# Kernel tuning notes

Hardware: AMD Instinct MI355X
Metric: run time of the kernel (lower is better)

Reference implementation:

```python
import jax, jax.numpy as jnp
import numpy as np

N = 40960      # nodes, level 0
E = 327680     # edges, level 0
N1 = 20480     # nodes after first graclus pool
E2 = 163840    # edges after first pool
N2 = 10240     # nodes after second graclus pool
B = 512        # graphs in batch
NCLS = 10


def seg_mean(v, idx, n):
    s = jax.ops.segment_sum(v, idx, num_segments=n)
    c = jax.ops.segment_sum(jnp.ones((idx.shape[0], 1), v.dtype), idx, num_segments=n)
    return s / jnp.maximum(c, 1.0)


def seg_max_f(v, idx, n):
    m = jax.ops.segment_max(v, idx, num_segments=n)
    return jnp.where(jnp.isneginf(m), 0.0, m)  # empty clusters -> 0


def cartesian(pos, ei):
    # PyG T.Cartesian(): cart = pos[row]-pos[col], normalized to [0,1]
    cart = pos[ei[0]] - pos[ei[1]]
    m = jnp.max(jnp.abs(cart))
    return cart / (2.0 * m) + 0.5


def nnconv_mean(x, ei, eattr, w1, b1, w2, b2, root, bias, n_nodes):
    # edge MLP -> per-edge weight matrix [E, Fin, Fout]
    fin, fout = root.shape
    h = jax.nn.relu(eattr @ w1 + b1) @ w2 + b2
    W = h.reshape(-1, fin, fout)
    src, dst = ei[0], ei[1]
    msg = jnp.einsum('ei,eio->eo', x[src], W)          # gather + per-edge matmul
    aggr = seg_mean(msg, dst, n_nodes)                 # scatter-mean
    return x @ root + aggr + bias


def setup_inputs() -> dict:
    key = jax.random.key(0)
    ks = jax.random.split(key, 24)
    inp = {}
    inp['x'] = jax.random.normal(ks[0], (N, 1), jnp.float32)
    inp['pos'] = jax.random.uniform(ks[1], (N, 2), jnp.float32) * 28.0
    inp['edge_attr'] = jax.random.uniform(ks[2], (E, 2), jnp.float32)
    inp['edge_index'] = jax.random.randint(ks[3], (2, E), 0, N)
    inp['batch'] = jnp.sort(jax.random.randint(ks[4], (N,), 0, B))
    inp['cluster1'] = jax.random.randint(ks[5], (N,), 0, N1)
    inp['edge_index2'] = jax.random.randint(ks[6], (2, E2), 0, N1)
    inp['cluster2'] = jax.random.randint(ks[7], (N1,), 0, N2)
    s = 0.1
    inp['nn1_w1'] = jax.random.normal(ks[8], (2, 25), jnp.float32) * s
    inp['nn1_b1'] = jnp.zeros((25,), jnp.float32)
    inp['nn1_w2'] = jax.random.normal(ks[9], (25, 32), jnp.float32) * s
    inp['nn1_b2'] = jnp.zeros((32,), jnp.float32)
    inp['root1'] = jax.random.normal(ks[10], (1, 32), jnp.float32) * s
    inp['bias1'] = jnp.zeros((32,), jnp.float32)
    inp['nn2_w1'] = jax.random.normal(ks[11], (2, 25), jnp.float32) * s
    inp['nn2_b1'] = jnp.zeros((25,), jnp.float32)
    inp['nn2_w2'] = jax.random.normal(ks[12], (25, 2048), jnp.float32) * s
    inp['nn2_b2'] = jnp.zeros((2048,), jnp.float32)
    inp['root2'] = jax.random.normal(ks[13], (32, 64), jnp.float32) * s
    inp['bias2'] = jnp.zeros((64,), jnp.float32)
    inp['fc1_w'] = jax.random.normal(ks[14], (64, 128), jnp.float32) * s
    inp['fc1_b'] = jnp.zeros((128,), jnp.float32)
    inp['fc2_w'] = jax.random.normal(ks[15], (128, NCLS), jnp.float32) * s
    inp['fc2_b'] = jnp.zeros((NCLS,), jnp.float32)
    return inp


def reference(x, pos, edge_attr, edge_index, batch, cluster1, edge_index2, cluster2,
              nn1_w1, nn1_b1, nn1_w2, nn1_b2, root1, bias1,
              nn2_w1, nn2_b1, nn2_w2, nn2_b2, root2, bias2,
              fc1_w, fc1_b, fc2_w, fc2_b):
    # conv1 + ELU
    x1 = jax.nn.elu(nnconv_mean(x, edge_index, edge_attr,
                                nn1_w1, nn1_b1, nn1_w2, nn1_b2, root1, bias1, N))
    # graclus max_pool (clusters precomputed): max features, mean pos, pooled batch
    x1p = seg_max_f(x1, cluster1, N1)
    pos1 = seg_mean(pos, cluster1, N1)
    batch1 = jnp.clip(jax.ops.segment_max(batch, cluster1, num_segments=N1), 0, B - 1)
    eattr2 = cartesian(pos1, edge_index2)  # transform=Cartesian on pooled graph
    # conv2 + ELU
    x2 = jax.nn.elu(nnconv_mean(x1p, edge_index2, eattr2,
                                nn2_w1, nn2_b1, nn2_w2, nn2_b2, root2, bias2, N1))
    # max_pool_x then global_mean_pool
    x2p = seg_max_f(x2, cluster2, N2)
    batch2 = jnp.clip(jax.ops.segment_max(batch1, cluster2, num_segments=N2), 0, B - 1)
    xg = seg_mean(x2p, batch2, B)
    h = jax.nn.elu(xg @ fc1_w + fc1_b)
    # dropout is identity in eval mode
    logits = h @ fc2_w + fc2_b
    return jax.nn.log_softmax(logits, axis=1)
```

## Files before the change

kernel.cpp:

```cpp
#include <hip/hip_runtime.h>
#include <hip/hip_bf16.h>
#include <limits.h>

#define NN   40960
#define EE   327680
#define NN1  20480
#define EE2  163840
#define NN2  10240
#define BB   512
#define NCLS 10

#define SEG1 160
#define SEG2 240
#define SEG3 320
#define SEG4 400
#define SBT  440

typedef short bf16x8 __attribute__((ext_vector_type(8)));
typedef float f32x4 __attribute__((ext_vector_type(4)));

__device__ __forceinline__ float elu_f(float v) { return v > 0.f ? v : (expf(v) - 1.f); }
__device__ __forceinline__ unsigned f2bf_bits(float v) {
    unsigned u = __float_as_uint(v);
    return (u + 0x7FFFu + ((u >> 16) & 1u)) >> 16;
}

__global__ void init_all(int* zbase, int zcount) {
    int i = blockIdx.x * 256 + threadIdx.x;
    if (i < zcount) zbase[i] = 0;
}

__global__ void deg_count(const int* __restrict__ ei, const int* __restrict__ ei2,
                          const int* __restrict__ cluster1, const int* __restrict__ cluster2,
                          int* deg1, int* degS, int* degD, int* degC1, int* degC2) {
    int i = blockIdx.x * 256 + threadIdx.x;
    if (i < EE) atomicAdd(deg1 + ei[EE + i], 1);
    if (i < EE2) {
        atomicAdd(degS + ei2[i], 1);
        atomicAdd(degD + ei2[EE2 + i], 1);
    }
    if (i < NN) atomicAdd(degC1 + cluster1[i], 1);
    if (i < NN1) atomicAdd(degC2 + cluster2[i], 1);
}

__global__ __launch_bounds__(256) void scan_partial(
    const int* __restrict__ deg1, const int* __restrict__ degS,
    const int* __restrict__ degD, const int* __restrict__ degC1,
    const int* __restrict__ degC2, int* __restrict__ part) {
    int b = blockIdx.x, t = threadIdx.x;
    const int* src;
    int off;
    if (b < SEG1)      { src = deg1;  off = b * 256; }
    else if (b < SEG2) { src = degS;  off = (b - SEG1) * 256; }
    else if (b < SEG3) { src = degD;  off = (b - SEG2) * 256; }
    else if (b < SEG4) { src = degC1; off = (b - SEG3) * 256; }
    else               { src = degC2; off = (b - SEG4) * 256; }
    int v = src[off + t];
#pragma unroll
    for (int o = 32; o; o >>= 1) v += __shfl_down(v, o, 64);
    __shared__ int sred[4];
    if ((t & 63) == 0) sred[t >> 6] = v;
    __syncthreads();
    if (t == 0) part[b] = sred[0] + sred[1] + sred[2] + sred[3];
}

__global__ void scan_base(const int* __restrict__ part, int* __restrict__ partBase,
                          int* rowptr1, int* rowptrS, int* rowptrD,
                          int* rowptrC1, int* rowptrC2) {
    __shared__ int sh[SBT];
    int t = threadIdx.x;
    if (t < SBT) sh[t] = part[t];
    __syncthreads();
    if (t < 5) {
        int lo[6] = {0, SEG1, SEG2, SEG3, SEG4, SBT};
        int run = 0;
        for (int b = lo[t]; b < lo[t + 1]; b++) { int v = sh[b]; sh[b] = run; run += v; }
    }
    if (t == 5) {
        rowptr1[NN] = EE;
        rowptrS[NN1] = EE2;
        rowptrD[NN1] = EE2;
        rowptrC1[NN1] = NN;
        rowptrC2[NN2] = NN1;
    }
    __syncthreads();
    if (t < SBT) partBase[t] = sh[t];
}

__global__ __launch_bounds__(256) void scan_apply(
    const int* __restrict__ deg1, const int* __restrict__ degS,
    const int* __restrict__ degD, const int* __restrict__ degC1,
    const int* __restrict__ degC2, const int* __restrict__ partBase,
    int* rowptr1, int* rowptrS, int* rowptrD, int* rowptrC1, int* rowptrC2,
    int* cur1, int* curS, int* curD, int* curC1, int* curC2) {
    int b = blockIdx.x, t = threadIdx.x;
    const int* src;
    int *rp, *cur;
    int off;
    if (b < SEG1)      { src = deg1;  rp = rowptr1;  cur = cur1;  off = b * 256; }
    else if (b < SEG2) { src = degS;  rp = rowptrS;  cur = curS;  off = (b - SEG1) * 256; }
    else if (b < SEG3) { src = degD;  rp = rowptrD;  cur = curD;  off = (b - SEG2) * 256; }
    else if (b < SEG4) { src = degC1; rp = rowptrC1; cur = curC1; off = (b - SEG3) * 256; }
    else               { src = degC2; rp = rowptrC2; cur = curC2; off = (b - SEG4) * 256; }
    __shared__ int sh[256];
    int v = src[off + t];
    sh[t] = v;
    __syncthreads();
#pragma unroll
    for (int o = 1; o < 256; o <<= 1) {
        int u = (t >= o) ? sh[t - o] : 0;
        __syncthreads();
        sh[t] += u;
        __syncthreads();
    }
    int excl = sh[t] - v + partBase[b];
    rp[off + t] = excl;
    cur[off + t] = excl;
}

__global__ void fill_csr(const float* __restrict__ x, const float* __restrict__ ea,
                         const int* __restrict__ ei, const int* __restrict__ ei2,
                         const int* __restrict__ cluster1, const int* __restrict__ cluster2,
                         int* cur1, int* curS, int* curD, int* curC1, int* curC2,
                         float4* eadj1, int* cscDst, int* cscSrc, int* dstFrom,
                         int* memC1, int* memC2) {
    int i = blockIdx.x * 256 + threadIdx.x;
    if (i < EE) {
        int s = ei[i], d = ei[EE + i];
        int p = atomicAdd(cur1 + d, 1);
        eadj1[p] = make_float4(x[s], ea[2 * i], ea[2 * i + 1], 0.f);
    }
    if (i < EE2) {
        int s2 = ei2[i], d2 = ei2[EE2 + i];
        int q = atomicAdd(curS + s2, 1);
        cscDst[q] = d2;
        cscSrc[q] = s2;
        int p2 = atomicAdd(curD + d2, 1);
        dstFrom[p2] = q;
    }
    if (i < NN) {
        int c = cluster1[i];
        int p = atomicAdd(curC1 + c, 1);
        memC1[p] = i;
    }
    if (i < NN1) {
        int c = cluster2[i];
        int p = atomicAdd(curC2 + c, 1);
        memC2[p] = i;
    }
}

__global__ __launch_bounds__(256) void conv1_gather(
    const float* __restrict__ x, const int* __restrict__ rowptr1,
    const float4* __restrict__ eadj1,
    const float* __restrict__ w1, const float* __restrict__ b1,
    const float* __restrict__ w2, const float* __restrict__ b2,
    const float* __restrict__ root1, const float* __restrict__ bias1,
    float* __restrict__ x1) {
    int t = threadIdx.x;
    int j = t & 31;
    int n = blockIdx.x * 8 + (t >> 5);
    float w1x = 0.f, w1y = 0.f, b1j = 0.f;
    if (j < 25) { w1x = w1[j]; w1y = w1[25 + j]; b1j = b1[j]; }
    int r0 = rowptr1[n], r1 = rowptr1[n + 1];
    float agg = 0.f, sumx = 0.f;
    float4 edN = (r0 < r1) ? eadj1[r0] : make_float4(0.f, 0.f, 0.f, 0.f);
    for (int p = r0; p < r1; p++) {
        float4 ed = edN;
        if (p + 1 < r1) edN = eadj1[p + 1];
        float h = fmaxf(fmaf(ed.y, w1x, fmaf(ed.z, w1y, b1j)), 0.f);
        agg = fmaf(ed.x, h, agg);
        sumx += ed.x;
    }
    float w2c[25];
#pragma unroll
    for (int k = 0; k < 25; k++) w2c[k] = w2[k * 32 + j];
    float m = sumx * b2[j];
#pragma unroll
    for (int k = 0; k < 25; k++) m = fmaf(__shfl(agg, k, 32), w2c[k], m);
    float deg = fmaxf((float)(r1 - r0), 1.f);
    float v = fmaf(x[n], root1[j], m / deg + bias1[j]);
    x1[(size_t)n * 32 + j] = elu_f(v);
}

__global__ __launch_bounds__(256) void pool1_gather(
    const float* __restrict__ x1, const float* __restrict__ pos,
    const int* __restrict__ batch, const int* __restrict__ rowptrC1,
    const int* __restrict__ memC1,
    float* __restrict__ x1p, float* __restrict__ pos1, int* __restrict__ batch1) {
    int t = threadIdx.x;
    int j = t & 31;
    int c = blockIdx.x * 8 + (t >> 5);
    int r0 = rowptrC1[c], r1 = rowptrC1[c + 1];
    float mx = -INFINITY, sx = 0.f, sy = 0.f;
    int bmax = INT_MIN;
    for (int p = r0; p < r1; p++) {
        int v = memC1[p];
        mx = fmaxf(mx, x1[(size_t)v * 32 + j]);
        bmax = max(bmax, batch[v]);
        if (j == 0) {
            float2 pv = ((const float2*)pos)[v];
            sx += pv.x; sy += pv.y;
        }
    }
    x1p[(size_t)c * 32 + j] = (r0 < r1) ? mx : 0.f;
    if (j == 0) {
        float cn = fmaxf((float)(r1 - r0), 1.f);
        pos1[2 * c] = sx / cn;
        pos1[2 * c + 1] = sy / cn;
        batch1[c] = min(max(bmax, 0), BB - 1);
    }
}

__global__ void cartmax(const float* __restrict__ pos1, const int* __restrict__ ei2,
                        unsigned* mBits, const float* __restrict__ x1p,
                        unsigned short* __restrict__ x1pb) {
    int e = blockIdx.x * 256 + threadIdx.x;
#pragma unroll
    for (int u = 0; u < 4; u++) {
        int idx = e * 4 + u;
        x1pb[idx] = (unsigned short)f2bf_bits(x1p[idx]);
    }
    float m = 0.f;
    if (e < EE2) {
        int r = ei2[e], c = ei2[EE2 + e];
        m = fmaxf(fabsf(pos1[2 * r] - pos1[2 * c]), fabsf(pos1[2 * r + 1] - pos1[2 * c + 1]));
    }
    for (int off = 32; off; off >>= 1) m = fmaxf(m, __shfl_xor(m, off, 64));
    if ((threadIdx.x & 63) == 0) atomicMax(mBits, __float_as_uint(m));
}

__global__ void prep_wext(const float* __restrict__ w2, const float* __restrict__ b2,
                          unsigned short* __restrict__ WextB) {
    int idx = blockIdx.x * 256 + threadIdx.x;
    if (idx >= 13 * 8 * 64 * 8) return;
    int j = idx & 7;
    int lane = (idx >> 3) & 63;
    int tile = (idx >> 9) & 7;
    int ky = idx >> 12;
    int h = tile >> 2, tt = tile & 3;
    int kmlp = 2 * ky + h;
    int o = tt * 16 + (lane & 15);
    int i = (lane >> 4) * 8 + j;
    float v = (kmlp < 25) ? w2[(size_t)kmlp * 2048 + i * 64 + o] : b2[i * 64 + o];
    WextB[idx] = (unsigned short)f2bf_bits(v);
}

__global__ __launch_bounds__(256) void a_gemm_mfma(
    const unsigned short* __restrict__ x1pb, const unsigned short* __restrict__ WextB,
    unsigned* __restrict__ Au) {
    int t = threadIdx.x;
    int lane = t & 63;
    int w = t >> 6;
    int ky = blockIdx.y;
    int m0 = blockIdx.x * 128 + w * 32;
    int lo16 = lane & 15, hi4 = lane >> 4;
    bf16x8 bf[8];
    const bf16x8* Bp = (const bf16x8*)(WextB + (size_t)ky * 4096);
#pragma unroll
    for (int i = 0; i < 8; i++) bf[i] = Bp[i * 64 + lane];
    const f32x4 zero = {0.f, 0.f, 0.f, 0.f};
#pragma unroll
    for (int mt = 0; mt < 2; mt++) {
        int mbase = m0 + mt * 16;
        bf16x8 af = *(const bf16x8*)(x1pb + ((size_t)(mbase + lo16) * 32 + hi4 * 8));
        f32x4 acc[8];
#pragma unroll
        for (int i = 0; i < 8; i++)
            acc[i] = __builtin_amdgcn_mfma_f32_16x16x32_bf16(af, bf[i], zero, 0, 0, 0);
#pragma unroll
        for (int tt = 0; tt < 4; tt++) {
#pragma unroll
            for (int j = 0; j < 4; j++) {
                int n = mbase + hi4 * 4 + j;
                unsigned lo = f2bf_bits(acc[tt][j]);
                unsigned hi = f2bf_bits(acc[4 + tt][j]);
                Au[(size_t)n * 832 + ky * 64 + tt * 16 + lo16] = lo | (hi << 16);
            }
        }
    }
}

__global__ __launch_bounds__(256) void r2_kernel(
    const int* __restrict__ cscSrc, const int* __restrict__ cscDst,
    const float* __restrict__ pos1, const float* __restrict__ w1,
    const float* __restrict__ b1, const unsigned* __restrict__ mBits,
    unsigned* __restrict__ r2) {
    int q = blockIdx.x * 256 + threadIdx.x;
    if (q >= EE2) return;
    int s = cscSrc[q], d = cscDst[q];
    float inv = 0.5f / __uint_as_float(*mBits);
    float2 ps = ((const float2*)pos1)[s];
    float2 pd = ((const float2*)pos1)[d];
    float cx = fmaf(ps.x - pd.x, inv, 0.5f);
    float cy = fmaf(ps.y - pd.y, inv, 0.5f);
    unsigned out[13];
#pragma unroll
    for (int ky = 0; ky < 13; ky++) {
        int k0 = 2 * ky, k1 = 2 * ky + 1;
        float rlo = fmaxf(fmaf(cx, w1[k0], fmaf(cy, w1[25 + k0], b1[k0])), 0.f);
        float rhi = 1.f;
        if (k1 < 25) rhi = fmaxf(fmaf(cx, w1[k1], fmaf(cy, w1[25 + k1], b1[k1])), 0.f);
        out[ky] = f2bf_bits(rlo) | (f2bf_bits(rhi) << 16);
    }
#pragma unroll
    for (int ky = 0; ky < 13; ky++) r2[(size_t)q * 13 + ky] = out[ky];
}

__global__ __launch_bounds__(256) void conv2_msg(
    const unsigned* __restrict__ Au, const unsigned* __restrict__ r2,
    const int* __restrict__ rowptrS, unsigned short* __restrict__ msgbuf) {
    int t = threadIdx.x;
    int lane = t & 63;
    int s = __builtin_amdgcn_readfirstlane(blockIdx.x * 4 + (t >> 6));
    unsigned au[13];
    const unsigned* Ab = Au + (size_t)s * 832 + lane;
#pragma unroll
    for (int ky = 0; ky < 13; ky++) au[ky] = Ab[ky * 64];
    int r0 = rowptrS[s], r1 = rowptrS[s + 1];
    for (int q = r0; q < r1; q++) {
        const unsigned* rr = r2 + (size_t)q * 13;
        float m0 = 0.f, m1 = 0.f;
#pragma unroll
        for (int ky = 0; ky < 13; ky++) {
            unsigned rp = rr[ky];
            unsigned ua = au[ky];
            m0 = fmaf(__uint_as_float(rp << 16), __uint_as_float(ua << 16), m0);
            m1 = fmaf(__uint_as_float(rp & 0xFFFF0000u), __uint_as_float(ua & 0xFFFF0000u), m1);
        }
        msgbuf[(size_t)q * 64 + lane] = (unsigned short)f2bf_bits(m0 + m1);
    }
}

__global__ __launch_bounds__(256) void conv2_fin(
    const unsigned short* __restrict__ msgbuf, const int* __restrict__ rowptrD,
    const int* __restrict__ dstFrom,
    const float* __restrict__ x1p, const float* __restrict__ root2,
    const float* __restrict__ bias2, float* __restrict__ x2) {
    int t = threadIdx.x;
    int lane = t & 63;
    int n = blockIdx.x * 4 + (t >> 6);
    float Rr[32];
#pragma unroll
    for (int i = 0; i < 32; i++) Rr[i] = root2[i * 64 + lane];
    int r0 = rowptrD[n], r1 = rowptrD[n + 1];
    float acc = 0.f;
    int qN = (r0 < r1) ? dstFrom[r0] : 0;
    for (int p = r0; p < r1; p++) {
        int q = qN;
        if (p + 1 < r1) qN = dstFrom[p + 1];
        acc += __uint_as_float((unsigned)msgbuf[(size_t)q * 64 + lane] << 16);
    }
    float deg = fmaxf((float)(r1 - r0), 1.f);
    float xv = x1p[(size_t)n * 32 + (lane & 31)];
    float ra2 = bias2[lane];
#pragma unroll
    for (int i = 0; i < 32; i++) ra2 = fmaf(__shfl(xv, i, 64), Rr[i], ra2);
    x2[(size_t)n * 64 + lane] = elu_f(ra2 + acc / deg);
}

__global__ __launch_bounds__(256) void pool2_gather(
    const float* __restrict__ x2, const int* __restrict__ rowptrC2,
    const int* __restrict__ memC2, const int* __restrict__ batch1,
    float* __restrict__ xgsumS, float* __restrict__ gcntS) {
    int t = threadIdx.x;
    int lane = t & 63;
    int n2 = blockIdx.x * 4 + (t >> 6);
    int r0 = rowptrC2[n2], r1 = rowptrC2[n2 + 1];
    float mx = -INFINITY;
    int bmax = INT_MIN;
    for (int p = r0; p < r1; p++) {
        int m = memC2[p];
        mx = fmaxf(mx, x2[(size_t)m * 64 + lane]);
        bmax = max(bmax, batch1[m]);
    }
    float v = (r0 < r1) ? mx : 0.f;
    int b = min(max(bmax, 0), BB - 1);
    int shard = n2 & 7;
    atomicAdd(xgsumS + ((size_t)shard * BB + b) * 64 + lane, v);
    if (lane == 0) atomicAdd(gcntS + shard * BB + b, 1.f);
}

__global__ __launch_bounds__(128) void head_kernel(
    const float* __restrict__ xgsumS, const float* __restrict__ gcntS,
    const float* __restrict__ fc1w, const float* __restrict__ fc1b,
    const float* __restrict__ fc2w, const float* __restrict__ fc2b,
    float* __restrict__ out) {
    int b = blockIdx.x;
    int t = threadIdx.x;
    __shared__ float xg[64];
    __shared__ float h[128];
    __shared__ float lg[NCLS];
    __shared__ float red[2];
    __shared__ float cntsh;
    float s = 0.f;
    if (t < 64) {
#pragma unroll
        for (int sh = 0; sh < 8; sh++) s += xgsumS[((size_t)sh * BB + b) * 64 + t];
    }
    if (t == 64) {
        float c = 0.f;
#pragma unroll
        for (int sh = 0; sh < 8; sh++) c += gcntS[sh * BB + b];
        cntsh = fmaxf(c, 1.f);
    }
    __syncthreads();
    if (t < 64) xg[t] = s / cntsh;
    __syncthreads();
    float a1 = fc1b[t];
    for (int i = 0; i < 64; i++) a1 = fmaf(xg[i], fc1w[i * 128 + t], a1);
    h[t] = elu_f(a1);
    __syncthreads();
    if (t < NCLS) {
        float a = fc2b[t];
        for (int j = 0; j < 128; j++) a = fmaf(h[j], fc2w[j * NCLS + t], a);
        lg[t] = a;
    }
    __syncthreads();
    if (t == 0) {
        float mx = lg[0];
        for (int i = 1; i < NCLS; i++) mx = fmaxf(mx, lg[i]);
        float se = 0.f;
        for (int i = 0; i < NCLS; i++) se += expf(lg[i] - mx);
        red[0] = mx;
        red[1] = logf(se);
    }
    __syncthreads();
    if (t < NCLS) out[(size_t)b * NCLS + t] = lg[t] - red[0] - red[1];
}

extern "C" void kernel_launch(void* const* d_in, const int* in_sizes, int n_in,
                              void* d_out, int out_size, void* d_ws, size_t ws_size,
                              hipStream_t stream) {
    const float* x = (const float*)d_in[0];
    const float* pos = (const float*)d_in[1];
    const float* edge_attr = (const float*)d_in[2];
    const int* ei = (const int*)d_in[3];
    const int* batch = (const int*)d_in[4];
    const int* cluster1 = (const int*)d_in[5];
    const int* ei2 = (const int*)d_in[6];
    const int* cluster2 = (const int*)d_in[7];
    const float* nn1_w1 = (const float*)d_in[8];
    const float* nn1_b1 = (const float*)d_in[9];
    const float* nn1_w2 = (const float*)d_in[10];
    const float* nn1_b2 = (const float*)d_in[11];
    const float* root1 = (const float*)d_in[12];
    const float* bias1 = (const float*)d_in[13];
    const float* nn2_w1 = (const float*)d_in[14];
    const float* nn2_b1 = (const float*)d_in[15];
    const float* nn2_w2 = (const float*)d_in[16];
    const float* nn2_b2 = (const float*)d_in[17];
    const float* root2 = (const float*)d_in[18];
    const float* bias2 = (const float*)d_in[19];
    const float* fc1w = (const float*)d_in[20];
    const float* fc1b = (const float*)d_in[21];
    const float* fc2w = (const float*)d_in[22];
    const float* fc2b = (const float*)d_in[23];

    float* ws = (float*)d_ws;
    constexpr size_t OFF_DEG1 = 0;
    constexpr size_t OFF_DEGS = OFF_DEG1 + NN;
    constexpr size_t OFF_DEGD = OFF_DEGS + NN1;
    constexpr size_t OFF_DEGC1 = OFF_DEGD + NN1;
    constexpr size_t OFF_DEGC2 = OFF_DEGC1 + NN1;
    constexpr size_t OFF_XGS = OFF_DEGC2 + NN2;
    constexpr size_t OFF_GCS = OFF_XGS + (size_t)8 * BB * 64;
    constexpr size_t OFF_MBITS = OFF_GCS + 8 * BB;
    constexpr size_t ZTOT = OFF_MBITS + 1;
    constexpr size_t OFF_PART = ZTOT;
    constexpr size_t OFF_PBASE = OFF_PART + SBT;
    constexpr size_t OFF_ROWPTR1 = OFF_PBASE + SBT;
    constexpr size_t OFF_ROWPTRS = OFF_ROWPTR1 + NN + 4;
    constexpr size_t OFF_ROWPTRD = OFF_ROWPTRS + NN1 + 4;
    constexpr size_t OFF_ROWPTRC1 = OFF_ROWPTRD + NN1 + 4;
    constexpr size_t OFF_ROWPTRC2 = OFF_ROWPTRC1 + NN1 + 4;
    constexpr size_t OFF_CUR1 = OFF_ROWPTRC2 + NN2 + 4;
    constexpr size_t OFF_CURS = OFF_CUR1 + NN;
    constexpr size_t OFF_CURD = OFF_CURS + NN1;
    constexpr size_t OFF_CURC1 = OFF_CURD + NN1;
    constexpr size_t OFF_CURC2 = OFF_CURC1 + NN1;
    constexpr size_t OFF_CSCDST = OFF_CURC2 + NN2;
    constexpr size_t OFF_CSCSRC = OFF_CSCDST + EE2;
    constexpr size_t OFF_DSTFROM = OFF_CSCSRC + EE2;
    constexpr size_t OFF_MEMC1 = OFF_DSTFROM + EE2;
    constexpr size_t OFF_MEMC2 = OFF_MEMC1 + NN;
    constexpr size_t OFF_X1 = OFF_MEMC2 + NN1;
    constexpr size_t OFF_X1P = OFF_X1 + (size_t)NN * 32;
    constexpr size_t OFF_X1PB = OFF_X1P + (size_t)NN1 * 32;
    constexpr size_t OFF_POS1 = OFF_X1PB + (size_t)NN1 * 16;
    constexpr size_t OFF_BATCH1 = OFF_POS1 + (size_t)NN1 * 2;
    constexpr size_t OFF_X2 = OFF_BATCH1 + NN1;
    constexpr size_t OFF_WEXTB = OFF_X2 + (size_t)NN1 * 64;
    constexpr size_t OFF_UA = OFF_WEXTB + 26624;
    constexpr size_t UASZ = (size_t)EE2 * 13;
    constexpr size_t OFF_MSG = OFF_UA + UASZ;
    constexpr size_t OFF_AU = OFF_MSG + (size_t)EE2 * 32;

    int* deg1 = (int*)(ws + OFF_DEG1);
    int* degS = (int*)(ws + OFF_DEGS);
    int* degD = (int*)(ws + OFF_DEGD);
    int* degC1 = (int*)(ws + OFF_DEGC1);
    int* degC2 = (int*)(ws + OFF_DEGC2);
    float* xgsumS = ws + OFF_XGS;
    float* gcntS = ws + OFF_GCS;
    unsigned* mBits = (unsigned*)(ws + OFF_MBITS);
    int* part = (int*)(ws + OFF_PART);
    int* partBase = (int*)(ws + OFF_PBASE);
    int* rowptr1 = (int*)(ws + OFF_ROWPTR1);
    int* rowptrS = (int*)(ws + OFF_ROWPTRS);
    int* rowptrD = (int*)(ws + OFF_ROWPTRD);
    int* rowptrC1 = (int*)(ws + OFF_ROWPTRC1);
    int* rowptrC2 = (int*)(ws + OFF_ROWPTRC2);
    int* cur1 = (int*)(ws + OFF_CUR1);
    int* curS = (int*)(ws + OFF_CURS);
    int* curD = (int*)(ws + OFF_CURD);
    int* curC1 = (int*)(ws + OFF_CURC1);
    int* curC2 = (int*)(ws + OFF_CURC2);
    int* cscDst = (int*)(ws + OFF_CSCDST);
    int* cscSrc = (int*)(ws + OFF_CSCSRC);
    int* dstFrom = (int*)(ws + OFF_DSTFROM);
    int* memC1 = (int*)(ws + OFF_MEMC1);
    int* memC2 = (int*)(ws + OFF_MEMC2);
    float* x1 = ws + OFF_X1;
    float* x1p = ws + OFF_X1P;
    unsigned short* x1pb = (unsigned short*)(ws + OFF_X1PB);
    float* pos1 = ws + OFF_POS1;
    int* batch1 = (int*)(ws + OFF_BATCH1);
    float* x2 = ws + OFF_X2;
    unsigned short* WextB = (unsigned short*)(ws + OFF_WEXTB);
    float4* eadj1 = (float4*)(ws + OFF_UA);
    unsigned* r2 = (unsigned*)(ws + OFF_UA);
    unsigned short* msgbuf = (unsigned short*)(ws + OFF_MSG);
    unsigned* Au = (unsigned*)(ws + OFF_AU);

    init_all<<<(int)((ZTOT + 255) / 256), 256, 0, stream>>>((int*)d_ws, (int)ZTOT);
    deg_count<<<EE / 256, 256, 0, stream>>>(ei, ei2, cluster1, cluster2,
                                            deg1, degS, degD, degC1, degC2);
    scan_partial<<<SBT, 256, 0, stream>>>(deg1, degS, degD, degC1, degC2, part);
    scan_base<<<1, 512, 0, stream>>>(part, partBase, rowptr1, rowptrS, rowptrD,
                                     rowptrC1, rowptrC2);
    scan_apply<<<SBT, 256, 0, stream>>>(deg1, degS, degD, degC1, degC2, partBase,
                                        rowptr1, rowptrS, rowptrD, rowptrC1, rowptrC2,
                                        cur1, curS, curD, curC1, curC2);
    fill_csr<<<EE / 256, 256, 0, stream>>>(x, edge_attr, ei, ei2, cluster1, cluster2,
                                           cur1, curS, curD, curC1, curC2,
                                           eadj1, cscDst, cscSrc, dstFrom, memC1, memC2);
    prep_wext<<<208, 256, 0, stream>>>(nn2_w2, nn2_b2, WextB);
    conv1_gather<<<NN / 8, 256, 0, stream>>>(x, rowptr1, eadj1,
                                             nn1_w1, nn1_b1, nn1_w2, nn1_b2, root1, bias1, x1);
    pool1_gather<<<NN1 / 8, 256, 0, stream>>>(x1, pos, batch, rowptrC1, memC1,
                                              x1p, pos1, batch1);
    cartmax<<<EE2 / 256, 256, 0, stream>>>(pos1, ei2, mBits, x1p, x1pb);
    a_gemm_mfma<<<dim3(NN1 / 128, 13), 256, 0, stream>>>(x1pb, WextB, Au);
    r2_kernel<<<EE2 / 256, 256, 0, stream>>>(cscSrc, cscDst, pos1, nn2_w1, nn2_b1, mBits, r2);
    conv2_msg<<<NN1 / 4, 256, 0, stream>>>(Au, r2, rowptrS, msgbuf);
    conv2_fin<<<NN1 / 4, 256, 0, stream>>>(msgbuf, rowptrD, dstFrom, x1p, root2, bias2, x2);
    pool2_gather<<<NN2 / 4, 256, 0, stream>>>(x2, rowptrC2, memC2, batch1, xgsumS, gcntS);
    head_kernel<<<BB, 128, 0, stream>>>(xgsumS, gcntS, fc1w, fc1b, fc2w, fc2b,
                                        (float*)d_out);
}
```

Measured before the change: 245.7 us.

## Record atomic slots in degree pass, scatter messages directly in dst order

The degree-count kernel now saves each element's atomic return value as its slot, so CSR fill becomes a plain rowptr+slot write with no second round of atomics and no cursor arrays. Edge source, destination and destination position are packed into one int4 record, and the per-edge r2 row is padded to 16 words so it can be read with vector loads and carry the destination slot. conv2_msg then writes messages straight into destination order, which removes the dstFrom indirection in conv2_fin. In exchange it adds slot arrays and padding that raise memory traffic, and the message writes become scattered instead of sequential.

New measurement: 208.9 us. -15.0%, faster.

```diff
diff --git a/kernel.cpp b/kernel.cpp
--- a/kernel.cpp
+++ b/kernel.cpp
@@ -32,15 +32,16 @@
 
 __global__ void deg_count(const int* __restrict__ ei, const int* __restrict__ ei2,
                           const int* __restrict__ cluster1, const int* __restrict__ cluster2,
-                          int* deg1, int* degS, int* degD, int* degC1, int* degC2) {
+                          int* deg1, int* degS, int* degD, int* degC1, int* degC2,
+                          int* slot1, int* slotS, int* slotD, int* slotC1, int* slotC2) {
     int i = blockIdx.x * 256 + threadIdx.x;
-    if (i < EE) atomicAdd(deg1 + ei[EE + i], 1);
+    if (i < EE) slot1[i] = atomicAdd(deg1 + ei[EE + i], 1);
     if (i < EE2) {
-        atomicAdd(degS + ei2[i], 1);
-        atomicAdd(degD + ei2[EE2 + i], 1);
-    }
-    if (i < NN) atomicAdd(degC1 + cluster1[i], 1);
-    if (i < NN1) atomicAdd(degC2 + cluster2[i], 1);
+        slotS[i] = atomicAdd(degS + ei2[i], 1);
+        slotD[i] = atomicAdd(degD + ei2[EE2 + i], 1);
+    }
+    if (i < NN) slotC1[i] = atomicAdd(degC1 + cluster1[i], 1);
+    if (i < NN1) slotC2[i] = atomicAdd(degC2 + cluster2[i], 1);
 }
 
 __global__ __launch_bounds__(256) void scan_partial(
@@ -91,17 +92,16 @@
     const int* __restrict__ deg1, const int* __restrict__ degS,
     const int* __restrict__ degD, const int* __restrict__ degC1,
     const int* __restrict__ degC2, const int* __restrict__ partBase,
-    int* rowptr1, int* rowptrS, int* rowptrD, int* rowptrC1, int* rowptrC2,
-    int* cur1, int* curS, int* curD, int* curC1, int* curC2) {
+    int* rowptr1, int* rowptrS, int* rowptrD, int* rowptrC1, int* rowptrC2) {
     int b = blockIdx.x, t = threadIdx.x;
     const int* src;
-    int *rp, *cur;
+    int* rp;
     int off;
-    if (b < SEG1)      { src = deg1;  rp = rowptr1;  cur = cur1;  off = b * 256; }
-    else if (b < SEG2) { src = degS;  rp = rowptrS;  cur = curS;  off = (b - SEG1) * 256; }
-    else if (b < SEG3) { src = degD;  rp = rowptrD;  cur = curD;  off = (b - SEG2) * 256; }
-    else if (b < SEG4) { src = degC1; rp = rowptrC1; cur = curC1; off = (b - SEG3) * 256; }
-    else               { src = degC2; rp = rowptrC2; cur = curC2; off = (b - SEG4) * 256; }
+    if (b < SEG1)      { src = deg1;  rp = rowptr1;  off = b * 256; }
+    else if (b < SEG2) { src = degS;  rp = rowptrS;  off = (b - SEG1) * 256; }
+    else if (b < SEG3) { src = degD;  rp = rowptrD;  off = (b - SEG2) * 256; }
+    else if (b < SEG4) { src = degC1; rp = rowptrC1; off = (b - SEG3) * 256; }
+    else               { src = degC2; rp = rowptrC2; off = (b - SEG4) * 256; }
     __shared__ int sh[256];
     int v = src[off + t];
     sh[t] = v;
@@ -113,41 +113,33 @@
         sh[t] += u;
         __syncthreads();
     }
-    int excl = sh[t] - v + partBase[b];
-    rp[off + t] = excl;
-    cur[off + t] = excl;
+    rp[off + t] = sh[t] - v + partBase[b];
 }
 
 __global__ void fill_csr(const float* __restrict__ x, const float* __restrict__ ea,
                          const int* __restrict__ ei, const int* __restrict__ ei2,
                          const int* __restrict__ cluster1, const int* __restrict__ cluster2,
-                         int* cur1, int* curS, int* curD, int* curC1, int* curC2,
-                         float4* eadj1, int* cscDst, int* cscSrc, int* dstFrom,
-                         int* memC1, int* memC2) {
+                         const int* __restrict__ rowptr1, const int* __restrict__ rowptrS,
+                         const int* __restrict__ rowptrD, const int* __restrict__ rowptrC1,
+                         const int* __restrict__ rowptrC2,
+                         const int* __restrict__ slot1, const int* __restrict__ slotS,
+                         const int* __restrict__ slotD, const int* __restrict__ slotC1,
+                         const int* __restrict__ slotC2,
+                         float4* __restrict__ eadj1, int4* __restrict__ cscRec,
+                         int* __restrict__ memC1, int* __restrict__ memC2) {
     int i = blockIdx.x * 256 + threadIdx.x;
     if (i < EE) {
         int s = ei[i], d = ei[EE + i];
-        int p = atomicAdd(cur1 + d, 1);
-        eadj1[p] = make_float4(x[s], ea[2 * i], ea[2 * i + 1], 0.f);
+        eadj1[rowptr1[d] + slot1[i]] = make_float4(x[s], ea[2 * i], ea[2 * i + 1], 0.f);
     }
     if (i < EE2) {
         int s2 = ei2[i], d2 = ei2[EE2 + i];
-        int q = atomicAdd(curS + s2, 1);
-        cscDst[q] = d2;
-        cscSrc[q] = s2;
-        int p2 = atomicAdd(curD + d2, 1);
-        dstFrom[p2] = q;
-    }
-    if (i < NN) {
-        int c = cluster1[i];
-        int p = atomicAdd(curC1 + c, 1);
-        memC1[p] = i;
-    }
-    if (i < NN1) {
-        int c = cluster2[i];
-        int p = atomicAdd(curC2 + c, 1);
-        memC2[p] = i;
-    }
+        int q = rowptrS[s2] + slotS[i];
+        int p2 = rowptrD[d2] + slotD[i];
+        cscRec[q] = make_int4(s2, d2, p2, 0);
+    }
+    if (i < NN) memC1[rowptrC1[cluster1[i]] + slotC1[i]] = i;
+    if (i < NN1) memC2[rowptrC2[cluster2[i]] + slotC2[i]] = i;
 }
 
 __global__ __launch_bounds__(256) void conv1_gather(
@@ -282,19 +274,19 @@
 }
 
 __global__ __launch_bounds__(256) void r2_kernel(
-    const int* __restrict__ cscSrc, const int* __restrict__ cscDst,
-    const float* __restrict__ pos1, const float* __restrict__ w1,
-    const float* __restrict__ b1, const unsigned* __restrict__ mBits,
-    unsigned* __restrict__ r2) {
+    const int4* __restrict__ cscRec, const float* __restrict__ pos1,
+    const float* __restrict__ w1, const float* __restrict__ b1,
+    const unsigned* __restrict__ mBits, uint4* __restrict__ r2q) {
     int q = blockIdx.x * 256 + threadIdx.x;
     if (q >= EE2) return;
-    int s = cscSrc[q], d = cscDst[q];
+    int4 rec = cscRec[q];
+    int s = rec.x, d = rec.y;
     float inv = 0.5f / __uint_as_float(*mBits);
     float2 ps = ((const float2*)pos1)[s];
     float2 pd = ((const float2*)pos1)[d];
     float cx = fmaf(ps.x - pd.x, inv, 0.5f);
     float cy = fmaf(ps.y - pd.y, inv, 0.5f);
-    unsigned out[13];
+    unsigned out[16];
 #pragma unroll
     for (int ky = 0; ky < 13; ky++) {
         int k0 = 2 * ky, k1 = 2 * ky + 1;
@@ -303,12 +295,17 @@
         if (k1 < 25) rhi = fmaxf(fmaf(cx, w1[k1], fmaf(cy, w1[25 + k1], b1[k1])), 0.f);
         out[ky] = f2bf_bits(rlo) | (f2bf_bits(rhi) << 16);
     }
-#pragma unroll
-    for (int ky = 0; ky < 13; ky++) r2[(size_t)q * 13 + ky] = out[ky];
+    out[13] = (unsigned)rec.z;
+    out[14] = 0u; out[15] = 0u;
+    uint4* dst = r2q + (size_t)q * 4;
+    dst[0] = make_uint4(out[0], out[1], out[2], out[3]);
+    dst[1] = make_uint4(out[4], out[5], out[6], out[7]);
+    dst[2] = make_uint4(out[8], out[9], out[10], out[11]);
+    dst[3] = make_uint4(out[12], out[13], out[14], out[15]);
 }
 
 __global__ __launch_bounds__(256) void conv2_msg(
-    const unsigned* __restrict__ Au, const unsigned* __restrict__ r2,
+    const unsigned* __restrict__ Au, const uint4* __restrict__ r2q,
     const int* __restrict__ rowptrS, unsigned short* __restrict__ msgbuf) {
     int t = threadIdx.x;
     int lane = t & 63;
@@ -319,7 +316,10 @@
     for (int ky = 0; ky < 13; ky++) au[ky] = Ab[ky * 64];
     int r0 = rowptrS[s], r1 = rowptrS[s + 1];
     for (int q = r0; q < r1; q++) {
-        const unsigned* rr = r2 + (size_t)q * 13;
+        const uint4* rp4 = r2q + (size_t)q * 4;
+        uint4 a = rp4[0], b = rp4[1], c = rp4[2], dd = rp4[3];
+        unsigned rr[13] = {a.x, a.y, a.z, a.w, b.x, b.y, b.z, b.w, c.x, c.y, c.z, c.w, dd.x};
+        unsigned dstSlot = dd.y;
         float m0 = 0.f, m1 = 0.f;
 #pragma unroll
         for (int ky = 0; ky < 13; ky++) {
@@ -328,13 +328,12 @@
             m0 = fmaf(__uint_as_float(rp << 16), __uint_as_float(ua << 16), m0);
             m1 = fmaf(__uint_as_float(rp & 0xFFFF0000u), __uint_as_float(ua & 0xFFFF0000u), m1);
         }
-        msgbuf[(size_t)q * 64 + lane] = (unsigned short)f2bf_bits(m0 + m1);
+        msgbuf[(size_t)dstSlot * 64 + lane] = (unsigned short)f2bf_bits(m0 + m1);
     }
 }
 
 __global__ __launch_bounds__(256) void conv2_fin(
     const unsigned short* __restrict__ msgbuf, const int* __restrict__ rowptrD,
-    const int* __restrict__ dstFrom,
     const float* __restrict__ x1p, const float* __restrict__ root2,
     const float* __restrict__ bias2, float* __restrict__ x2) {
     int t = threadIdx.x;
@@ -345,12 +344,8 @@
     for (int i = 0; i < 32; i++) Rr[i] = root2[i * 64 + lane];
     int r0 = rowptrD[n], r1 = rowptrD[n + 1];
     float acc = 0.f;
-    int qN = (r0 < r1) ? dstFrom[r0] : 0;
-    for (int p = r0; p < r1; p++) {
-        int q = qN;
-        if (p + 1 < r1) qN = dstFrom[p + 1];
-        acc += __uint_as_float((unsigned)msgbuf[(size_t)q * 64 + lane] << 16);
-    }
+    for (int p = r0; p < r1; p++)
+        acc += __uint_as_float((unsigned)msgbuf[(size_t)p * 64 + lane] << 16);
     float deg = fmaxf((float)(r1 - r0), 1.f);
     float xv = x1p[(size_t)n * 32 + (lane & 31)];
     float ra2 = bias2[lane];
@@ -466,7 +461,7 @@
     constexpr size_t OFF_XGS = OFF_DEGC2 + NN2;
     constexpr size_t OFF_GCS = OFF_XGS + (size_t)8 * BB * 64;
     constexpr size_t OFF_MBITS = OFF_GCS + 8 * BB;
-    constexpr size_t ZTOT = OFF_MBITS + 1;
+    constexpr size_t ZTOT = OFF_MBITS + 4;
     constexpr size_t OFF_PART = ZTOT;
     constexpr size_t OFF_PBASE = OFF_PART + SBT;
     constexpr size_t OFF_ROWPTR1 = OFF_PBASE + SBT;
@@ -474,15 +469,13 @@
     constexpr size_t OFF_ROWPTRD = OFF_ROWPTRS + NN1 + 4;
     constexpr size_t OFF_ROWPTRC1 = OFF_ROWPTRD + NN1 + 4;
     constexpr size_t OFF_ROWPTRC2 = OFF_ROWPTRC1 + NN1 + 4;
-    constexpr size_t OFF_CUR1 = OFF_ROWPTRC2 + NN2 + 4;
-    constexpr size_t OFF_CURS = OFF_CUR1 + NN;
-    constexpr size_t OFF_CURD = OFF_CURS + NN1;
-    constexpr size_t OFF_CURC1 = OFF_CURD + NN1;
-    constexpr size_t OFF_CURC2 = OFF_CURC1 + NN1;
-    constexpr size_t OFF_CSCDST = OFF_CURC2 + NN2;
-    constexpr size_t OFF_CSCSRC = OFF_CSCDST + EE2;
-    constexpr size_t OFF_DSTFROM = OFF_CSCSRC + EE2;
-    constexpr size_t OFF_MEMC1 = OFF_DSTFROM + EE2;
+    constexpr size_t OFF_SLOT1 = OFF_ROWPTRC2 + NN2 + 4;
+    constexpr size_t OFF_SLOTS = OFF_SLOT1 + EE;
+    constexpr size_t OFF_SLOTD = OFF_SLOTS + EE2;
+    constexpr size_t OFF_SLOTC1 = OFF_SLOTD + EE2;
+    constexpr size_t OFF_SLOTC2 = OFF_SLOTC1 + NN;
+    constexpr size_t OFF_CSCREC = OFF_SLOTC2 + NN1;
+    constexpr size_t OFF_MEMC1 = OFF_CSCREC + (size_t)EE2 * 4;
     constexpr size_t OFF_MEMC2 = OFF_MEMC1 + NN;
     constexpr size_t OFF_X1 = OFF_MEMC2 + NN1;
     constexpr size_t OFF_X1P = OFF_X1 + (size_t)NN * 32;
@@ -492,7 +485,7 @@
     constexpr size_t OFF_X2 = OFF_BATCH1 + NN1;
     constexpr size_t OFF_WEXTB = OFF_X2 + (size_t)NN1 * 64;
     constexpr size_t OFF_UA = OFF_WEXTB + 26624;
-    constexpr size_t UASZ = (size_t)EE2 * 13;
+    constexpr size_t UASZ = (size_t)EE2 * 16;
     constexpr size_t OFF_MSG = OFF_UA + UASZ;
     constexpr size_t OFF_AU = OFF_MSG + (size_t)EE2 * 32;
 
@@ -511,14 +504,12 @@
     int* rowptrD = (int*)(ws + OFF_ROWPTRD);
     int* rowptrC1 = (int*)(ws + OFF_ROWPTRC1);
     int* rowptrC2 = (int*)(ws + OFF_ROWPTRC2);
-    int* cur1 = (int*)(ws + OFF_CUR1);
-    int* curS = (int*)(ws + OFF_CURS);
-    int* curD = (int*)(ws + OFF_CURD);
-    int* curC1 = (int*)(ws + OFF_CURC1);
-    int* curC2 = (int*)(ws + OFF_CURC2);
-    int* cscDst = (int*)(ws + OFF_CSCDST);
-    int* cscSrc = (int*)(ws + OFF_CSCSRC);
-    int* dstFrom = (int*)(ws + OFF_DSTFROM);
+    int* slot1 = (int*)(ws + OFF_SLOT1);
+    int* slotS = (int*)(ws + OFF_SLOTS);
+    int* slotD = (int*)(ws + OFF_SLOTD);
+    int* slotC1 = (int*)(ws + OFF_SLOTC1);
+    int* slotC2 = (int*)(ws + OFF_SLOTC2);
+    int4* cscRec = (int4*)(ws + OFF_CSCREC);
     int* memC1 = (int*)(ws + OFF_MEMC1);
     int* memC2 = (int*)(ws + OFF_MEMC2);
     float* x1 = ws + OFF_X1;
@@ -529,22 +520,23 @@
     float* x2 = ws + OFF_X2;
     unsigned short* WextB = (unsigned short*)(ws + OFF_WEXTB);
     float4* eadj1 = (float4*)(ws + OFF_UA);
-    unsigned* r2 = (unsigned*)(ws + OFF_UA);
+    uint4* r2q = (uint4*)(ws + OFF_UA);
     unsigned short* msgbuf = (unsigned short*)(ws + OFF_MSG);
     unsigned* Au = (unsigned*)(ws + OFF_AU);
 
     init_all<<<(int)((ZTOT + 255) / 256), 256, 0, stream>>>((int*)d_ws, (int)ZTOT);
     deg_count<<<EE / 256, 256, 0, stream>>>(ei, ei2, cluster1, cluster2,
-                                            deg1, degS, degD, degC1, degC2);
+                                            deg1, degS, degD, degC1, degC2,
+                                            slot1, slotS, slotD, slotC1, slotC2);
     scan_partial<<<SBT, 256, 0, stream>>>(deg1, degS, degD, degC1, degC2, part);
     scan_base<<<1, 512, 0, stream>>>(part, partBase, rowptr1, rowptrS, rowptrD,
                                      rowptrC1, rowptrC2);
     scan_apply<<<SBT, 256, 0, stream>>>(deg1, degS, degD, degC1, degC2, partBase,
-                                        rowptr1, rowptrS, rowptrD, rowptrC1, rowptrC2,
-                                        cur1, curS, curD, curC1, curC2);
+                                        rowptr1, rowptrS, rowptrD, rowptrC1, rowptrC2);
     fill_csr<<<EE / 256, 256, 0, stream>>>(x, edge_attr, ei, ei2, cluster1, cluster2,
-                                           cur1, curS, curD, curC1, curC2,
-                                           eadj1, cscDst, cscSrc, dstFrom, memC1, memC2);
+                                           rowptr1, rowptrS, rowptrD, rowptrC1, rowptrC2,
+                                           slot1, slotS, slotD, slotC1, slotC2,
+                                           eadj1, cscRec, memC1, memC2);
     prep_wext<<<208, 256, 0, stream>>>(nn2_w2, nn2_b2, WextB);
     conv1_gather<<<NN / 8, 256, 0, stream>>>(x, rowptr1, eadj1,
                                              nn1_w1, nn1_b1, nn1_w2, nn1_b2, root1, bias1, x1);
@@ -552,9 +544,9 @@
                                               x1p, pos1, batch1);
     cartmax<<<EE2 / 256, 256, 0, stream>>>(pos1, ei2, mBits, x1p, x1pb);
     a_gemm_mfma<<<dim3(NN1 / 128, 13), 256, 0, stream>>>(x1pb, WextB, Au);
-    r2_kernel<<<EE2 / 256, 256, 0, stream>>>(cscSrc, cscDst, pos1, nn2_w1, nn2_b1, mBits, r2);
-    conv2_msg<<<NN1 / 4, 256, 0, stream>>>(Au, r2, rowptrS, msgbuf);
-    conv2_fin<<<NN1 / 4, 256, 0, stream>>>(msgbuf, rowptrD, dstFrom, x1p, root2, bias2, x2);
+    r2_kernel<<<EE2 / 256, 256, 0, stream>>>(cscRec, pos1, nn2_w1, nn2_b1, mBits, r2q);
+    conv2_msg<<<NN1 / 4, 256, 0, stream>>>(Au, r2q, rowptrS, msgbuf);
+    conv2_fin<<<NN1 / 4, 256, 0, stream>>>(msgbuf, rowptrD, x1p, root2, bias2, x2);
     pool2_gather<<<NN2 / 4, 256, 0, stream>>>(x2, rowptrC2, memC2, batch1, xgsumS, gcntS);
     head_kernel<<<BB, 128, 0, stream>>>(xgsumS, gcntS, fc1w, fc1b, fc2w, fc2b,
                                         (float*)d_out);
```
